# Performance work log

Hardware: AMD Instinct MI355X
Metric: run time of the kernel (lower is better)

Reference implementation:

```python
import jax, jax.numpy as jnp
import numpy as np

N_LAYERS = 4
D_IN = 64
D_OUT = 64
D_MODEL = 512
D_STATE = 256
RMIN, RMAX, MAX_PHASE = 0.8, 0.95, 2.0 * np.pi


def setup_inputs() -> dict:
    key = jax.random.key(0)
    rng = np.random.default_rng(0)
    B, L = 8, 2048
    u = jax.random.normal(key, (B, L, D_IN), dtype=jnp.float32)
    # encoder/decoder (nn.Linear, bias=False): weight shape [out, in]
    encoder_w = jnp.asarray(rng.standard_normal((D_MODEL, D_IN)) / np.sqrt(D_IN), jnp.float32)
    decoder_w = jnp.asarray(rng.standard_normal((D_OUT, D_MODEL)) / np.sqrt(D_MODEL), jnp.float32)
    # LRU params per block (standard ring init on eigenvalues)
    u1 = rng.uniform(size=(N_LAYERS, D_STATE))
    u2 = rng.uniform(size=(N_LAYERS, D_STATE))
    nu_log = jnp.asarray(np.log(-0.5 * np.log(u1 * (RMAX**2 - RMIN**2) + RMIN**2)), jnp.float32)
    theta_log = jnp.asarray(np.log(MAX_PHASE * u2), jnp.float32)
    B_re = jnp.asarray(rng.standard_normal((N_LAYERS, D_STATE, D_MODEL)) / np.sqrt(2 * D_MODEL), jnp.float32)
    B_im = jnp.asarray(rng.standard_normal((N_LAYERS, D_STATE, D_MODEL)) / np.sqrt(2 * D_MODEL), jnp.float32)
    C_re = jnp.asarray(rng.standard_normal((N_LAYERS, D_MODEL, D_STATE)) / np.sqrt(D_STATE), jnp.float32)
    C_im = jnp.asarray(rng.standard_normal((N_LAYERS, D_MODEL, D_STATE)) / np.sqrt(D_STATE), jnp.float32)
    D = jnp.asarray(rng.standard_normal((N_LAYERS, D_MODEL)), jnp.float32)
    # GLU feedforward: y = (x W1^T) * sigmoid(x W2^T)
    W1 = jnp.asarray(rng.standard_normal((N_LAYERS, D_MODEL, D_MODEL)) / np.sqrt(D_MODEL), jnp.float32)
    W2 = jnp.asarray(rng.standard_normal((N_LAYERS, D_MODEL, D_MODEL)) / np.sqrt(D_MODEL), jnp.float32)
    res_logit = jnp.full((N_LAYERS,), -1.0, jnp.float32)
    return dict(u=u, encoder_w=encoder_w, decoder_w=decoder_w, nu_log=nu_log,
                theta_log=theta_log, B_re=B_re, B_im=B_im, C_re=C_re, C_im=C_im,
                D=D, W1=W1, W2=W2, res_logit=res_logit)


def _lru(x, nu, th, Bre, Bim, Cre, Cim, Dv):
    # diagonal complex LRU: h_t = lam*h_{t-1} + gamma*B u_t ; y = Re(C h) + D*u
    lam = jnp.exp(-jnp.exp(nu) + 1j * jnp.exp(th)).astype(jnp.complex64)  # [N]
    gam = jnp.sqrt(1.0 - jnp.abs(lam) ** 2).astype(jnp.complex64)
    Bc = (Bre + 1j * Bim).astype(jnp.complex64)  # [N, D]
    Bu = jnp.einsum('bld,nd->bln', x.astype(jnp.complex64), Bc) * gam  # [B,L,N]
    lam_b = jnp.broadcast_to(lam, Bu.shape)

    def comb(a, b):
        return (a[0] * b[0], a[1] * b[0] + b[1])

    _, h = jax.lax.associative_scan(comb, (lam_b, Bu), axis=1)
    Cc = (Cre + 1j * Cim).astype(jnp.complex64)  # [D, N]
    return jnp.real(jnp.einsum('bln,dn->bld', h, Cc)) + Dv * x


def reference(u, encoder_w, decoder_w, nu_log, theta_log, B_re, B_im, C_re, C_im, D, W1, W2, res_logit):
    x = jnp.einsum('bli,mi->blm', u, encoder_w)  # encoder
    for k in range(N_LAYERS):
        z = _lru(x, nu_log[k], theta_log[k], B_re[k], B_im[k], C_re[k], C_im[k], D[k])
        z = jnp.einsum('bld,od->blo', z, W1[k]) * jax.nn.sigmoid(jnp.einsum('bld,od->blo', z, W2[k]))
        x = x + jax.nn.sigmoid(res_logit[k]) * z  # gated residual (dropout=0)
    return jnp.einsum('blm,om->blo', x, decoder_w)  # decoder
```

## Files before the change

### kernel.cpp

```cpp
#include <hip/hip_runtime.h>
#include <cmath>

#define DM 512
#define DS 256
#define NL 4
#define BATCH 8
#define SEQ 2048
#define MROWS (BATCH*SEQ)
#define LCH 32
#define NCH 64

typedef unsigned short ushort_t;
typedef unsigned int uint_t;
typedef __attribute__((ext_vector_type(8))) short short8;
typedef __attribute__((ext_vector_type(4))) float floatx4;

__device__ __forceinline__ float sigmoidf_(float v) { return 1.0f / (1.0f + __expf(-v)); }

__device__ __forceinline__ ushort_t f2bf(float f) {
    union { float f; unsigned int u; } c; c.f = f;
    unsigned int u = c.u;
    u += 0x7fffu + ((u >> 16) & 1u);
    return (ushort_t)(u >> 16);
}
__device__ __forceinline__ float bf2f(uint_t h) {
    union { unsigned int u; float f; } c; c.u = (h & 0xffffu) << 16; return c.f;
}
__device__ __forceinline__ uint_t pack2(float a, float b) {
    return (uint_t)f2bf(a) | ((uint_t)f2bf(b) << 16);
}

#define AS1 __attribute__((address_space(1)))
#define AS3 __attribute__((address_space(3)))
__device__ __forceinline__ void gl_lds16(const void* g, void* l) {
    __builtin_amdgcn_global_load_lds((const AS1 uint_t*)g, (AS3 uint_t*)l, 16, 0, 0);
}

struct GemmArgs {
    const ushort_t* A;
    const ushort_t* Wa;
    const ushort_t* Wb;
    const ushort_t* xbf_in;
    const float* gam;
    const float* Dv;
    float* of32;
    ushort_t* obf;
    float* xf32;
    const float* resp;
    int K;
    int N;
    int layer;
};

#define PREFETCH_TILE(it_, buf_)                                                        \
    do {                                                                                \
        const size_t kb_ = (size_t)(it_) * 64;                                          \
        char* dst_ = smem + (buf_) * HALF;                                              \
        gl_lds16(Ap + (size_t)(wid * 16 + lrow) * Kb + kb_, dst_ + wid * 1024);         \
        gl_lds16(Ap + (size_t)((wid + 4) * 16 + lrow) * Kb + kb_,                       \
                 dst_ + (wid + 4) * 1024);                                              \
        gl_lds16(B0p + (size_t)(wid * 16 + lrow) * Kb + kb_, dst_ + AB + wid * 1024);   \
        if constexpr (BN == 128) {                                                      \
            gl_lds16(B0p + (size_t)((wid + 4) * 16 + lrow) * Kb + kb_,                  \
                     dst_ + AB + (wid + 4) * 1024);                                     \
        }                                                                               \
        if constexpr (DUAL) {                                                           \
            gl_lds16(B1p + (size_t)(wid * 16 + lrow) * Kb + kb_,                        \
                     dst_ + AB + BB + wid * 1024);                                      \
            gl_lds16(B1p + (size_t)((wid + 4) * 16 + lrow) * Kb + kb_,                  \
                     dst_ + AB + BB + (wid + 4) * 1024);                                \
        }                                                                               \
    } while (0)

template<int BN, int EPI, int DUAL>
__launch_bounds__(256, DUAL ? 2 : 3)
__global__ void mgemm(const GemmArgs p) {
    constexpr int BM = 128;
    constexpr int MT = (BN == 128) ? 4 : 2;
    constexpr int NT = 4;
    constexpr int WROWS = MT * 16;
    constexpr int AB = 8192;
    constexpr int BB = (BN == 128) ? 8192 : 4096;
    constexpr int B1B = DUAL ? 8192 : 0;
    constexpr int HALF = AB + BB + B1B;
    constexpr int EPB = (EPI == 4) ? 0 : 32 * 132 * 4;
    constexpr int SMB = (2 * HALF > EPB) ? 2 * HALF : EPB;
    __shared__ __align__(16) char smem[SMB];

    const int K = p.K, N = p.N;
    const int tid = threadIdx.x, lane = tid & 63, wid = tid >> 6;
    const int wm = (BN == 128) ? (wid & 1) : wid;
    const int wn = (BN == 128) ? (wid >> 1) : 0;
    const int m0 = blockIdx.x * BM, n0 = blockIdx.y * BN;
    const int q = lane >> 4, r16 = lane & 15;
    const int lrow = lane >> 2;
    const size_t Kb = (size_t)K * 2;
    const char* Ap  = (const char*)p.A  + (size_t)m0 * Kb + (lane & 3) * 16;
    const char* B0p = (const char*)p.Wa + (size_t)n0 * Kb + (lane & 3) * 16;
    const char* B1p = (const char*)p.Wb + (size_t)n0 * Kb + (lane & 3) * 16;

    floatx4 acc0[MT][NT] = {};
    floatx4 acc1[DUAL ? MT : 1][DUAL ? NT : 1] = {};

    const int iters = K >> 5;
    PREFETCH_TILE(0, 0);
    for (int it = 0; it < iters; ++it) {
        __syncthreads();
        if (it + 1 < iters) PREFETCH_TILE(it + 1, (it + 1) & 1);
        const ushort_t* As  = (const ushort_t*)(smem + (it & 1) * HALF);
        const ushort_t* Bs0 = (const ushort_t*)(smem + (it & 1) * HALF + AB);
        const ushort_t* Bs1 = (const ushort_t*)(smem + (it & 1) * HALF + AB + BB);

        short8 af[MT], b0[NT], b1[DUAL ? NT : 1];
#pragma unroll
        for (int i = 0; i < MT; ++i)
            af[i] = *(const short8*)&As[(wm * WROWS + i * 16 + r16) * 32 + q * 8];
#pragma unroll
        for (int j = 0; j < NT; ++j) {
            b0[j] = *(const short8*)&Bs0[(wn * 64 + j * 16 + r16) * 32 + q * 8];
            if constexpr (DUAL)
                b1[j] = *(const short8*)&Bs1[(wn * 64 + j * 16 + r16) * 32 + q * 8];
        }
#pragma unroll
        for (int i = 0; i < MT; ++i)
#pragma unroll
            for (int j = 0; j < NT; ++j) {
                acc0[i][j] = __builtin_amdgcn_mfma_f32_16x16x32_bf16(af[i], b0[j], acc0[i][j], 0, 0, 0);
                if constexpr (DUAL)
                    acc1[i][j] = __builtin_amdgcn_mfma_f32_16x16x32_bf16(af[i], b1[j], acc1[i][j], 0, 0, 0);
            }
    }

    if constexpr (EPI == 4) {
#pragma unroll
        for (int i = 0; i < MT; ++i)
#pragma unroll
            for (int j = 0; j < NT; ++j)
#pragma unroll
                for (int rr = 0; rr < 4; ++rr) {
                    const int row = m0 + wm * WROWS + i * 16 + q * 4 + rr;
                    const int col = wn * 64 + j * 16 + r16;
                    p.of32[(size_t)row * N + col] = acc0[i][j][rr];
                }
        return;
    } else {
        float* eps = (float*)smem;
        float rsv = 0.f;
        if constexpr (EPI == 3) rsv = sigmoidf_(p.resp[p.layer]);

#pragma unroll
        for (int i = 0; i < MT; ++i) {
            __syncthreads();
#pragma unroll
            for (int j = 0; j < NT; ++j) {
                const int colt = wn * 64 + j * 16 + r16;
#pragma unroll
                for (int rr = 0; rr < 4; ++rr) {
                    float v = acc0[i][j][rr];
                    if constexpr (EPI == 1) v *= p.gam[(n0 + colt) >> 1];
                    if constexpr (EPI == 3) v = rsv * v * sigmoidf_(acc1[i][j][rr]);
                    eps[(wm * 16 + q * 4 + rr) * 132 + colt] = v;
                }
            }
            __syncthreads();
            const int row_r = tid >> 3, colg = (tid & 7) * 16;
            const int grow = m0 + (row_r >> 4) * 64 + i * 16 + (row_r & 15);
            const int gcol = n0 + colg;
            float4 f[4];
#pragma unroll
            for (int c = 0; c < 4; ++c) f[c] = *(float4*)&eps[row_r * 132 + colg + c * 4];
            const size_t ob = (size_t)grow * N + gcol;

            if constexpr (EPI == 0) {
#pragma unroll
                for (int c = 0; c < 4; ++c) *(float4*)(p.of32 + ob + c * 4) = f[c];
            } else if constexpr (EPI == 2) {
                uint_t xp[8];
                *(uint4*)(xp)     = *(const uint4*)(p.xbf_in + ob);
                *(uint4*)(xp + 4) = *(const uint4*)(p.xbf_in + ob + 8);
#pragma unroll
                for (int c = 0; c < 4; ++c) {
                    float4 dv = *(const float4*)(p.Dv + gcol + c * 4);
                    f[c].x += dv.x * bf2f(xp[2 * c]);
                    f[c].y += dv.y * bf2f(xp[2 * c] >> 16);
                    f[c].z += dv.z * bf2f(xp[2 * c + 1]);
                    f[c].w += dv.w * bf2f(xp[2 * c + 1] >> 16);
                }
            } else if constexpr (EPI == 3) {
#pragma unroll
                for (int c = 0; c < 4; ++c) {
                    float4 xv = *(const float4*)(p.xf32 + ob + c * 4);
                    f[c].x += xv.x; f[c].y += xv.y; f[c].z += xv.z; f[c].w += xv.w;
                    *(float4*)(p.xf32 + ob + c * 4) = f[c];
                }
            }
            uint4 p0, p1;
            p0.x = pack2(f[0].x, f[0].y); p0.y = pack2(f[0].z, f[0].w);
            p0.z = pack2(f[1].x, f[1].y); p0.w = pack2(f[1].z, f[1].w);
            p1.x = pack2(f[2].x, f[2].y); p1.y = pack2(f[2].z, f[2].w);
            p1.z = pack2(f[3].x, f[3].y); p1.w = pack2(f[3].z, f[3].w);
            *(uint4*)(p.obf + ob) = p0;
            *(uint4*)(p.obf + ob + 8) = p1;
        }
    }
}

__global__ void prep_w(const float* __restrict__ Bre, const float* __restrict__ Bim,
                       const float* __restrict__ Cre, const float* __restrict__ Cim,
                       const float* __restrict__ W1, const float* __restrict__ W2,
                       const float* __restrict__ enc, const float* __restrict__ dec,
                       ushort_t* __restrict__ WBb, ushort_t* __restrict__ Wzb,
                       ushort_t* __restrict__ W1b, ushort_t* __restrict__ W2b,
                       ushort_t* __restrict__ encb, ushort_t* __restrict__ decb) {
    const int idx = blockIdx.x * 256 + threadIdx.x;
    const int k = idx & 511, n = (idx >> 9) & 511, l = idx >> 18;
    {
        const int s = n >> 1, part = n & 1;
        const float* src = part ? Bim : Bre;
        WBb[idx] = f2bf(src[((size_t)l * DS + s) * DM + k]);
    }
    {
        const int s = k >> 1, part = k & 1;
        float v = part ? -Cim[((size_t)l * DM + n) * DS + s]
                       :  Cre[((size_t)l * DM + n) * DS + s];
        Wzb[idx] = f2bf(v);
    }
    W1b[idx] = f2bf(W1[idx]);
    W2b[idx] = f2bf(W2[idx]);
    if (idx < DM * 64) { encb[idx] = f2bf(enc[idx]); decb[idx] = f2bf(dec[idx]); }
}

__global__ void prep_u(const float* __restrict__ u, ushort_t* __restrict__ ubf) {
    const int idx = blockIdx.x * 256 + threadIdx.x;
    ubf[idx] = f2bf(u[idx]);
}

__global__ void prep_tab(const float* __restrict__ nu, const float* __restrict__ th,
                         float* __restrict__ lre, float* __restrict__ lim,
                         float* __restrict__ gm) {
    const int idx = blockIdx.x * 256 + threadIdx.x;
    float a = expf(-expf(nu[idx])), t = expf(th[idx]);
    lre[idx] = a * cosf(t);
    lim[idx] = a * sinf(t);
    gm[idx] = sqrtf(fmaxf(0.f, 1.f - a * a));
}

__global__ void scan_ends(const uint_t* __restrict__ Bu, const float* __restrict__ lre_,
                          const float* __restrict__ lim_, float* __restrict__ carry) {
    const int s = threadIdx.x;
    const int blk = blockIdx.x, b = blk >> 6, c = blk & 63;
    const float lre = lre_[s], lim = lim_[s];
    float hre = 0.f, him = 0.f;
    size_t base = ((size_t)b * SEQ + (size_t)c * LCH) * DS + s;
#pragma unroll 8
    for (int i = 0; i < LCH; ++i, base += DS) {
        uint_t u = Bu[base];
        float br = bf2f(u), bi = bf2f(u >> 16);
        float nr = fmaf(lre, hre, fmaf(-lim, him, br));
        float ni = fmaf(lre, him, fmaf(lim, hre, bi));
        hre = nr; him = ni;
    }
    carry[(size_t)blk * 512 + s] = hre;
    carry[(size_t)blk * 512 + DS + s] = him;
}

__global__ void scan_carry(float* __restrict__ carry, const float* __restrict__ lre_,
                           const float* __restrict__ lim_) {
    const int s = threadIdx.x, b = blockIdx.x;
    float pre = lre_[s], pim = lim_[s];
    for (int t = 0; t < 5; ++t) {
        float nr = pre * pre - pim * pim, ni = 2.f * pre * pim;
        pre = nr; pim = ni;
    }
    size_t base = (size_t)b * NCH * 512 + s;
    float gre = carry[base], gim = carry[base + DS];
    for (int c = 1; c < NCH; ++c) {
        size_t id = base + (size_t)c * 512;
        float cr = carry[id], ci = carry[id + DS];
        float nr = fmaf(pre, gre, fmaf(-pim, gim, cr));
        float ni = fmaf(pre, gim, fmaf(pim, gre, ci));
        gre = nr; gim = ni;
        carry[id] = gre; carry[id + DS] = gim;
    }
}

__global__ void scan_apply(const uint_t* __restrict__ Bu, const float* __restrict__ lre_,
                           const float* __restrict__ lim_, const float* __restrict__ carry,
                           uint_t* __restrict__ h) {
    const int s = threadIdx.x;
    const int blk = blockIdx.x, b = blk >> 6, c = blk & 63;
    const float lre = lre_[s], lim = lim_[s];
    float hre = 0.f, him = 0.f;
    if (c > 0) {
        size_t cb = (size_t)(blk - 1) * 512 + s;
        hre = carry[cb]; him = carry[cb + DS];
    }
    size_t base = ((size_t)b * SEQ + (size_t)c * LCH) * DS + s;
#pragma unroll 8
    for (int i = 0; i < LCH; ++i, base += DS) {
        uint_t u = Bu[base];
        float br = bf2f(u), bi = bf2f(u >> 16);
        float nr = fmaf(lre, hre, fmaf(-lim, him, br));
        float ni = fmaf(lre, him, fmaf(lim, hre, bi));
        hre = nr; him = ni;
        h[base] = pack2(hre, him);
    }
}

extern "C" void kernel_launch(void* const* d_in, const int* in_sizes, int n_in,
                              void* d_out, int out_size, void* d_ws, size_t ws_size,
                              hipStream_t stream) {
    const float* u   = (const float*)d_in[0];
    const float* enc = (const float*)d_in[1];
    const float* dec = (const float*)d_in[2];
    const float* nu  = (const float*)d_in[3];
    const float* th  = (const float*)d_in[4];
    const float* Bre = (const float*)d_in[5];
    const float* Bim = (const float*)d_in[6];
    const float* Cre = (const float*)d_in[7];
    const float* Cim = (const float*)d_in[8];
    const float* Dp  = (const float*)d_in[9];
    const float* W1  = (const float*)d_in[10];
    const float* W2  = (const float*)d_in[11];
    const float* res = (const float*)d_in[12];
    float* out = (float*)d_out;

    const size_t MD = (size_t)MROWS * DM;
    float* x     = (float*)d_ws;
    float* carry = x + MD;
    float* lre   = carry + (size_t)BATCH * NCH * 512;
    float* lim   = lre + NL * DS;
    float* gmt   = lim + NL * DS;
    ushort_t* xbf  = (ushort_t*)(gmt + NL * DS);
    ushort_t* Bubf = xbf + MD;
    ushort_t* hbf  = Bubf + MD;
    ushort_t* zbf  = hbf + MD;
    ushort_t* ubf  = zbf;
    ushort_t* WBb  = zbf + MD;
    ushort_t* Wzb  = WBb + (size_t)NL * DM * DM;
    ushort_t* W1b  = Wzb + (size_t)NL * DM * DM;
    ushort_t* W2b  = W1b + (size_t)NL * DM * DM;
    ushort_t* encb = W2b + (size_t)NL * DM * DM;
    ushort_t* decb = encb + DM * 64;

    prep_w<<<NL * DM * DM / 256, 256, 0, stream>>>(Bre, Bim, Cre, Cim, W1, W2, enc, dec,
                                                   WBb, Wzb, W1b, W2b, encb, decb);
    prep_u<<<MROWS * 64 / 256, 256, 0, stream>>>(u, ubf);
    prep_tab<<<NL, 256, 0, stream>>>(nu, th, lre, lim, gmt);

    const dim3 gFull(MROWS / 128, DM / 128);

    {
        GemmArgs a = {};
        a.A = ubf; a.Wa = encb; a.K = 64; a.N = DM;
        a.of32 = x; a.obf = xbf;
        mgemm<128, 0, 0><<<gFull, 256, 0, stream>>>(a);
    }

    for (int k = 0; k < NL; ++k) {
        {
            GemmArgs a = {};
            a.A = xbf; a.Wa = WBb + (size_t)k * DM * DM; a.K = DM; a.N = DM;
            a.obf = Bubf; a.gam = gmt + k * DS;
            mgemm<128, 1, 0><<<gFull, 256, 0, stream>>>(a);
        }
        scan_ends<<<BATCH * NCH, 256, 0, stream>>>((const uint_t*)Bubf,
                                                   lre + k * DS, lim + k * DS, carry);
        scan_carry<<<BATCH, 256, 0, stream>>>(carry, lre + k * DS, lim + k * DS);
        scan_apply<<<BATCH * NCH, 256, 0, stream>>>((const uint_t*)Bubf,
                                                    lre + k * DS, lim + k * DS, carry,
                                                    (uint_t*)hbf);
        {
            GemmArgs a = {};
            a.A = hbf; a.Wa = Wzb + (size_t)k * DM * DM; a.K = DM; a.N = DM;
            a.obf = zbf; a.xbf_in = xbf; a.Dv = Dp + k * DM;
            mgemm<128, 2, 0><<<gFull, 256, 0, stream>>>(a);
        }
        {
            GemmArgs a = {};
            a.A = zbf; a.Wa = W1b + (size_t)k * DM * DM; a.Wb = W2b + (size_t)k * DM * DM;
            a.K = DM; a.N = DM;
            a.obf = xbf; a.xf32 = x; a.resp = res; a.layer = k;
            mgemm<128, 3, 1><<<gFull, 256, 0, stream>>>(a);
        }
    }
    {
        GemmArgs a = {};
        a.A = xbf; a.Wa = decb; a.K = DM; a.N = 64;
        a.of32 = out;
        mgemm<64, 4, 0><<<dim3(MROWS / 128, 1), 256, 0, stream>>>(a);
    }
}
```

Before: 426.2 us.

## Fuse chunk-end scan into Bu GEMM epilogue and drop separate scan passes

Computes each 32-row chunk's local scan end state inside the Bu GEMM epilogue from the fp32 staging tile in LDS, removing the scan_ends kernel that re-read Bu. The carry-propagation kernel is removed too: scan_apply now folds all previous chunk ends serially, using lambda^32, to get its starting state. The three prep kernels are merged into one. This saves a full read of Bu and two launches per layer. In exchange, later chunks in scan_apply do up to 63 serial dependent steps, and the ends are taken from fp32 values before bf16 rounding.

Result: slower. 462.0 us (+8.4%).

```diff
diff --git a/kernel.cpp b/kernel.cpp
--- a/kernel.cpp
+++ b/kernel.cpp
@@ -43,6 +43,9 @@
     const ushort_t* xbf_in;
     const float* gam;
     const float* Dv;
+    const float* lre;
+    const float* lim;
+    float* ends;
     float* of32;
     ushort_t* obf;
     float* xf32;
@@ -148,6 +151,17 @@
         float rsv = 0.f;
         if constexpr (EPI == 3) rsv = sigmoidf_(p.resp[p.layer]);
 
+        float sre = 0.f, sim = 0.f, lamr = 0.f, lami = 0.f;
+        int sg = 0, bidx = 0, cbase = 0;
+        if constexpr (EPI == 1) {
+            if (tid < 128) {
+                sg = (n0 >> 1) + (tid & 63);
+                lamr = p.lre[sg]; lami = p.lim[sg];
+                bidx = m0 >> 11;
+                cbase = (m0 & 2047) >> 5;
+            }
+        }
+
 #pragma unroll
         for (int i = 0; i < MT; ++i) {
             __syncthreads();
@@ -201,17 +215,43 @@
             p1.z = pack2(f[3].x, f[3].y); p1.w = pack2(f[3].z, f[3].w);
             *(uint4*)(p.obf + ob) = p0;
             *(uint4*)(p.obf + ob + 8) = p1;
-        }
-    }
-}
-
-__global__ void prep_w(const float* __restrict__ Bre, const float* __restrict__ Bim,
-                       const float* __restrict__ Cre, const float* __restrict__ Cim,
-                       const float* __restrict__ W1, const float* __restrict__ W2,
-                       const float* __restrict__ enc, const float* __restrict__ dec,
-                       ushort_t* __restrict__ WBb, ushort_t* __restrict__ Wzb,
-                       ushort_t* __restrict__ W1b, ushort_t* __restrict__ W2b,
-                       ushort_t* __restrict__ encb, ushort_t* __restrict__ decb) {
+
+            if constexpr (EPI == 1) {
+                if (tid < 128) {
+                    const int rbase = (tid >> 6) * 16;
+                    const int pp = (tid & 63) * 2;
+#pragma unroll
+                    for (int r = 0; r < 16; ++r) {
+                        float br = eps[(rbase + r) * 132 + pp];
+                        float bi = eps[(rbase + r) * 132 + pp + 1];
+                        float nr = fmaf(lamr, sre, fmaf(-lami, sim, br));
+                        float ni = fmaf(lamr, sim, fmaf(lami, sre, bi));
+                        sre = nr; sim = ni;
+                    }
+                    if (i & 1) {
+                        const int cc = cbase + (tid >> 6) * 2 + (i >> 1);
+                        p.ends[((size_t)bidx * NCH + cc) * 512 + sg] = sre;
+                        p.ends[((size_t)bidx * NCH + cc) * 512 + DS + sg] = sim;
+                        sre = 0.f; sim = 0.f;
+                    }
+                }
+            }
+        }
+    }
+}
+
+__global__ void prep_all(const float* __restrict__ u, const float* __restrict__ enc,
+                         const float* __restrict__ dec, const float* __restrict__ nu,
+                         const float* __restrict__ th,
+                         const float* __restrict__ Bre, const float* __restrict__ Bim,
+                         const float* __restrict__ Cre, const float* __restrict__ Cim,
+                         const float* __restrict__ W1, const float* __restrict__ W2,
+                         ushort_t* __restrict__ WBb, ushort_t* __restrict__ Wzb,
+                         ushort_t* __restrict__ W1b, ushort_t* __restrict__ W2b,
+                         ushort_t* __restrict__ encb, ushort_t* __restrict__ decb,
+                         ushort_t* __restrict__ ubf,
+                         float* __restrict__ lre, float* __restrict__ lim,
+                         float* __restrict__ gm) {
     const int idx = blockIdx.x * 256 + threadIdx.x;
     const int k = idx & 511, n = (idx >> 9) & 511, l = idx >> 18;
     {
@@ -227,74 +267,37 @@
     }
     W1b[idx] = f2bf(W1[idx]);
     W2b[idx] = f2bf(W2[idx]);
+    ubf[idx] = f2bf(u[idx]);
     if (idx < DM * 64) { encb[idx] = f2bf(enc[idx]); decb[idx] = f2bf(dec[idx]); }
-}
-
-__global__ void prep_u(const float* __restrict__ u, ushort_t* __restrict__ ubf) {
-    const int idx = blockIdx.x * 256 + threadIdx.x;
-    ubf[idx] = f2bf(u[idx]);
-}
-
-__global__ void prep_tab(const float* __restrict__ nu, const float* __restrict__ th,
-                         float* __restrict__ lre, float* __restrict__ lim,
-                         float* __restrict__ gm) {
-    const int idx = blockIdx.x * 256 + threadIdx.x;
-    float a = expf(-expf(nu[idx])), t = expf(th[idx]);
-    lre[idx] = a * cosf(t);
-    lim[idx] = a * sinf(t);
-    gm[idx] = sqrtf(fmaxf(0.f, 1.f - a * a));
-}
-
-__global__ void scan_ends(const uint_t* __restrict__ Bu, const float* __restrict__ lre_,
-                          const float* __restrict__ lim_, float* __restrict__ carry) {
-    const int s = threadIdx.x;
-    const int blk = blockIdx.x, b = blk >> 6, c = blk & 63;
-    const float lre = lre_[s], lim = lim_[s];
-    float hre = 0.f, him = 0.f;
-    size_t base = ((size_t)b * SEQ + (size_t)c * LCH) * DS + s;
-#pragma unroll 8
-    for (int i = 0; i < LCH; ++i, base += DS) {
-        uint_t u = Bu[base];
-        float br = bf2f(u), bi = bf2f(u >> 16);
-        float nr = fmaf(lre, hre, fmaf(-lim, him, br));
-        float ni = fmaf(lre, him, fmaf(lim, hre, bi));
-        hre = nr; him = ni;
-    }
-    carry[(size_t)blk * 512 + s] = hre;
-    carry[(size_t)blk * 512 + DS + s] = him;
-}
-
-__global__ void scan_carry(float* __restrict__ carry, const float* __restrict__ lre_,
-                           const float* __restrict__ lim_) {
-    const int s = threadIdx.x, b = blockIdx.x;
-    float pre = lre_[s], pim = lim_[s];
-    for (int t = 0; t < 5; ++t) {
-        float nr = pre * pre - pim * pim, ni = 2.f * pre * pim;
-        pre = nr; pim = ni;
-    }
-    size_t base = (size_t)b * NCH * 512 + s;
-    float gre = carry[base], gim = carry[base + DS];
-    for (int c = 1; c < NCH; ++c) {
-        size_t id = base + (size_t)c * 512;
-        float cr = carry[id], ci = carry[id + DS];
-        float nr = fmaf(pre, gre, fmaf(-pim, gim, cr));
-        float ni = fmaf(pre, gim, fmaf(pim, gre, ci));
-        gre = nr; gim = ni;
-        carry[id] = gre; carry[id + DS] = gim;
+    if (idx < NL * DS) {
+        float a = expf(-expf(nu[idx])), t = expf(th[idx]);
+        lre[idx] = a * cosf(t);
+        lim[idx] = a * sinf(t);
+        gm[idx] = sqrtf(fmaxf(0.f, 1.f - a * a));
     }
 }
 
 __global__ void scan_apply(const uint_t* __restrict__ Bu, const float* __restrict__ lre_,
-                           const float* __restrict__ lim_, const float* __restrict__ carry,
+                           const float* __restrict__ lim_, const float* __restrict__ ends,
                            uint_t* __restrict__ h) {
     const int s = threadIdx.x;
     const int blk = blockIdx.x, b = blk >> 6, c = blk & 63;
     const float lre = lre_[s], lim = lim_[s];
-    float hre = 0.f, him = 0.f;
-    if (c > 0) {
-        size_t cb = (size_t)(blk - 1) * 512 + s;
-        hre = carry[cb]; him = carry[cb + DS];
-    }
+    float l32r = lre, l32i = lim;
+    for (int t = 0; t < 5; ++t) {
+        float nr = l32r * l32r - l32i * l32i, ni = 2.f * l32r * l32i;
+        l32r = nr; l32i = ni;
+    }
+    float gre = 0.f, gim = 0.f;
+    const size_t eb = (size_t)b * NCH * 512 + s;
+    for (int j = 0; j < c; ++j) {
+        float er = ends[eb + (size_t)j * 512];
+        float ei = ends[eb + (size_t)j * 512 + DS];
+        float nr = fmaf(l32r, gre, fmaf(-l32i, gim, er));
+        float ni = fmaf(l32r, gim, fmaf(l32i, gre, ei));
+        gre = nr; gim = ni;
+    }
+    float hre = gre, him = gim;
     size_t base = ((size_t)b * SEQ + (size_t)c * LCH) * DS + s;
 #pragma unroll 8
     for (int i = 0; i < LCH; ++i, base += DS) {
@@ -327,8 +330,8 @@
 
     const size_t MD = (size_t)MROWS * DM;
     float* x     = (float*)d_ws;
-    float* carry = x + MD;
-    float* lre   = carry + (size_t)BATCH * NCH * 512;
+    float* ends  = x + MD;
+    float* lre   = ends + (size_t)BATCH * NCH * 512;
     float* lim   = lre + NL * DS;
     float* gmt   = lim + NL * DS;
     ushort_t* xbf  = (ushort_t*)(gmt + NL * DS);
@@ -343,10 +346,9 @@
     ushort_t* encb = W2b + (size_t)NL * DM * DM;
     ushort_t* decb = encb + DM * 64;
 
-    prep_w<<<NL * DM * DM / 256, 256, 0, stream>>>(Bre, Bim, Cre, Cim, W1, W2, enc, dec,
-                                                   WBb, Wzb, W1b, W2b, encb, decb);
-    prep_u<<<MROWS * 64 / 256, 256, 0, stream>>>(u, ubf);
-    prep_tab<<<NL, 256, 0, stream>>>(nu, th, lre, lim, gmt);
+    prep_all<<<NL * DM * DM / 256, 256, 0, stream>>>(
+        u, enc, dec, nu, th, Bre, Bim, Cre, Cim, W1, W2,
+        WBb, Wzb, W1b, W2b, encb, decb, ubf, lre, lim, gmt);
 
     const dim3 gFull(MROWS / 128, DM / 128);
 
@@ -362,13 +364,11 @@
             GemmArgs a = {};
             a.A = xbf; a.Wa = WBb + (size_t)k * DM * DM; a.K = DM; a.N = DM;
             a.obf = Bubf; a.gam = gmt + k * DS;
+            a.lre = lre + k * DS; a.lim = lim + k * DS; a.ends = ends;
             mgemm<128, 1, 0><<<gFull, 256, 0, stream>>>(a);
         }
-        scan_ends<<<BATCH * NCH, 256, 0, stream>>>((const uint_t*)Bubf,
-                                                   lre + k * DS, lim + k * DS, carry);
-        scan_carry<<<BATCH, 256, 0, stream>>>(carry, lre + k * DS, lim + k * DS);
         scan_apply<<<BATCH * NCH, 256, 0, stream>>>((const uint_t*)Bubf,
-                                                    lre + k * DS, lim + k * DS, carry,
+                                                    lre + k * DS, lim + k * DS, ends,
                                                     (uint_t*)hbf);
         {
             GemmArgs a = {};
```
